# Kernel optimization log

Measured on AMD Instinct MI355X. Metric: run time of the kernel, lower is better.

The kernel has to match this reference:

```python
import jax, jax.numpy as jnp
import numpy as np

N = 100000   # nodes
E = 1600000  # edges (avg in-degree 16)
D = 64       # feature dim (dim_in = dim_out)


def setup_inputs() -> dict:
    key = jax.random.key(0)
    k1, k2, k3, k4, k5, k6 = jax.random.split(key, 6)
    h = jax.random.normal(k1, (N, D), dtype=jnp.float32)
    src = jax.random.randint(k2, (E,), 0, N, dtype=jnp.int32)
    dst = jax.random.randint(k3, (E,), 0, N, dtype=jnp.int32)
    scale = 1.0 / np.sqrt(D).astype(np.float32)
    W1 = jax.random.normal(k4, (D, D), dtype=jnp.float32) * scale  # Linear(dim_in, dim_out, bias=False)
    W2 = jax.random.normal(k5, (D, D), dtype=jnp.float32) * scale  # Linear(dim_out, dim_out, bias=True)
    b2 = jax.random.normal(k6, (D,), dtype=jnp.float32) * scale
    return {"h": h, "src": src, "dst": dst, "W1": W1, "W2": W2, "b2": b2}


def reference(h, src, dst, W1, W2, b2):
    # GINConv with 'max' aggregation, eps = 0 (DGL default, not learned):
    #   out = MLP( h + max_{(u->v) in E} h[u] )
    msgs = h[src]  # [E, D] gather of source features
    agg = jax.ops.segment_max(msgs, dst, num_segments=N)  # [N, D]
    # Nodes with no in-edges: DGL's max-reduce yields zeros, segment_max yields -inf.
    deg = jax.ops.segment_sum(jnp.ones((E,), dtype=h.dtype), dst, num_segments=N)  # [N]
    agg = jnp.where(deg[:, None] > 0, agg, jnp.zeros((), dtype=h.dtype))
    x = h + agg                       # (1 + eps) * h_dst + agg, eps = 0
    y = jnp.maximum(x @ W1.T, 0.0)    # Linear(no bias) + ReLU
    return y @ W2.T + b2              # Linear(bias)
```

## Files before the change

kernel.cpp:

```cpp
#include <hip/hip_runtime.h>
#include <math.h>

#define NN 100000
#define EE 1600000
#define D 64

#define CSH 9
#define CSIZE 512
#define NCB 196
#define CAPC 8800
#define GCS 16
#define BSH 7
#define BSIZE 128
#define NBUK 782
#define AST 65

#define EPB 2048
#define NCHUNK ((EE + EPB - 1) / EPB)
#define KPER (EPB / 256)
#define GRID 1024


__device__ __forceinline__ unsigned short encbf(float x) {
    unsigned int b = __float_as_uint(x);
    unsigned short u = (unsigned short)((b + 0x7FFFu + ((b >> 16) & 1u)) >> 16);
    return u ^ ((u & 0x8000u) ? 0xFFFFu : 0x8000u);
}

__device__ __forceinline__ unsigned int pkmax(unsigned int a, unsigned int b) {
    unsigned int d;
    asm("v_pk_max_u16 %0, %1, %2" : "=v"(d) : "v"(a), "v"(b));
    return d;
}

__global__ void __launch_bounds__(256) kAP2(const float* __restrict__ h,
                                            unsigned short* __restrict__ hb,
                                            const float* __restrict__ W1, float* __restrict__ W1T,
                                            const float* __restrict__ W2, float* __restrict__ W2T,
                                            const int* __restrict__ src, const int* __restrict__ dst,
                                            int* __restrict__ gcurC, int* __restrict__ bdataC) {
    __shared__ int lcnt[NCB];
    __shared__ int lofs[NCB];
    __shared__ int gb[NCB];
    __shared__ int lcur2[NCB];
    __shared__ unsigned int ent[EPB];
    __shared__ unsigned char bkb[EPB];
    const int t = threadIdx.x;
    const int b = blockIdx.x;

    if (b < NCHUNK) {
        for (int i = t; i < NCB; i += 256) lcnt[i] = 0;
        __syncthreads();
        const int e0 = b * EPB;
        int es[KPER], ed[KPER];
#pragma unroll
        for (int k = 0; k < KPER; k++) {
            int e = e0 + k * 256 + t;
            int d = -1, s = 0;
            if (e < EE) {
                d = dst[e];
                s = src[e];
                atomicAdd(&lcnt[d >> CSH], 1);
            }
            ed[k] = d; es[k] = s;
        }
        __syncthreads();
        if (t < NCB) lofs[t] = lcnt[t];
        __syncthreads();
        for (int s = 1; s < NCB; s <<= 1) {
            int v = 0;
            if (t < NCB) { v = lofs[t]; if (t >= s) v += lofs[t - s]; }
            __syncthreads();
            if (t < NCB) lofs[t] = v;
            __syncthreads();
        }
        if (t < NCB) {
            int c = lcnt[t];
            int ex = lofs[t] - c;
            lcur2[t] = ex;
            lofs[t] = ex;
            gb[t] = c ? atomicAdd(&gcurC[t * GCS], c) : 0;
        }
        __syncthreads();
#pragma unroll
        for (int k = 0; k < KPER; k++) {
            if (ed[k] >= 0) {
                int bk = ed[k] >> CSH;
                int p = atomicAdd(&lcur2[bk], 1);
                ent[p] = ((unsigned)es[k] << CSH) | (unsigned)(ed[k] & (CSIZE - 1));
                bkb[p] = (unsigned char)bk;
            }
        }
        __syncthreads();
        const int tot = (e0 + EPB <= EE) ? EPB : (EE - e0);
        for (int i = t; i < tot; i += 256) {
            int bk = bkb[i];
            int p = gb[bk] + (i - lofs[bk]);
            if (p < CAPC) bdataC[bk * CAPC + p] = (int)ent[i];
        }
    }

    const int gid = b * 256 + t;
    const int gsz = gridDim.x * 256;
    const float4* h4 = (const float4*)h;
    ushort4* hb4 = (ushort4*)hb;
    for (int idx = gid; idx < NN * D / 4; idx += gsz) {
        float4 v = h4[idx];
        ushort4 r;
        r.x = encbf(v.x); r.y = encbf(v.y); r.z = encbf(v.z); r.w = encbf(v.w);
        hb4[idx] = r;
    }
    if (gid < D * D) {
        int k = gid >> 6, j = gid & 63;
        W1T[gid] = W1[j * D + k];
        W2T[gid] = W2[j * D + k];
    }
}

__global__ void __launch_bounds__(512) kC3(const float* __restrict__ h,
                                           const unsigned short* __restrict__ hb,
                                           const int* __restrict__ gcurC,
                                           const int* __restrict__ bdataC,
                                           const float* __restrict__ W1T,
                                           const float* __restrict__ W2T,
                                           const float* __restrict__ b2,
                                           float* __restrict__ out) {
    __shared__ unsigned int acc[BSIZE * AST];
    __shared__ int deg[BSIZE];
    __shared__ int scn[BSIZE];
    __shared__ int cur[BSIZE];
    float* fac = (float*)acc;
    unsigned int* elist = acc;
    const int t = threadIdx.x;
    const int b = blockIdx.x;
    const int cb = b >> 2;
    const unsigned int sub = (unsigned)(b & 3);
    int cnt = gcurC[cb * GCS];
    if (cnt > CAPC) cnt = CAPC;
    const int cbase = cb * CAPC;

    if (t < BSIZE) deg[t] = 0;
    __syncthreads();
    for (int i = t; i < cnt; i += 512) {
        unsigned int e = (unsigned)bdataC[cbase + i];
        if (((e >> BSH) & 3u) == sub) atomicAdd(&deg[e & (BSIZE - 1)], 1);
    }
    __syncthreads();
    if (t < BSIZE) scn[t] = deg[t];
    __syncthreads();
    for (int s = 1; s < BSIZE; s <<= 1) {
        int v = 0;
        if (t < BSIZE) { v = scn[t]; if (t >= s) v += scn[t - s]; }
        __syncthreads();
        if (t < BSIZE) scn[t] = v;
        __syncthreads();
    }
    if (t < BSIZE) cur[t] = scn[t] - deg[t];
    __syncthreads();
    for (int i = t; i < cnt; i += 512) {
        unsigned int e = (unsigned)bdataC[cbase + i];
        if (((e >> BSH) & 3u) == sub) {
            int pos = atomicAdd(&cur[e & (BSIZE - 1)], 1);
            elist[pos] = e >> CSH;
        }
    }
    __syncthreads();

    const int wave = t >> 6, lane = t & 63;
    const int oct = lane >> 3;
    const int fbyte = (lane & 7) * 16;
    const char* hbB = (const char*)hb;
    unsigned int m[2][4];
#pragma unroll
    for (int p = 0; p < 2; ++p)
#pragma unroll
        for (int c = 0; c < 4; ++c) m[p][c] = 0u;

#pragma unroll
    for (int p = 0; p < 2; ++p) {
        const int n8 = wave * 16 + p * 8 + oct;
        const int dg = deg[n8];
        const int ofs = scn[n8] - dg;
        int md = dg;
        md = max(md, __shfl_xor(md, 8));
        md = max(md, __shfl_xor(md, 16));
        md = max(md, __shfl_xor(md, 32));
        for (int r0 = 0; r0 < md; r0 += 8) {
            uint4 u[8];
#pragma unroll
            for (int g = 0; g < 8; ++g) {
                int r = r0 + g;
                u[g] = make_uint4(0u, 0u, 0u, 0u);
                if (r < dg) {
                    unsigned int sidx = elist[ofs + r];
                    u[g] = *(const uint4*)(hbB + (size_t)sidx * 128 + fbyte);
                }
            }
#pragma unroll
            for (int g = 0; g < 8; ++g) {
                m[p][0] = pkmax(m[p][0], u[g].x);
                m[p][1] = pkmax(m[p][1], u[g].y);
                m[p][2] = pkmax(m[p][2], u[g].z);
                m[p][3] = pkmax(m[p][3], u[g].w);
            }
        }
    }
    __syncthreads();

#pragma unroll
    for (int p = 0; p < 2; ++p) {
        const int n8 = wave * 16 + p * 8 + oct;
        const int v = b * BSIZE + n8;
        const int f0 = (lane & 7) * 8;
        float x[8];
#pragma unroll
        for (int c = 0; c < 4; ++c) {
            unsigned int w = m[p][c];
            unsigned int klo = w & 0xFFFFu;
            unsigned int khi = w >> 16;
            float mlo = 0.0f, mhi = 0.0f;
            if (klo) {
                unsigned int bb = (klo & 0x8000u) ? (klo ^ 0x8000u) : ((~klo) & 0xFFFFu);
                mlo = __uint_as_float(bb << 16);
            }
            if (khi) {
                unsigned int bb = (khi & 0x8000u) ? (khi ^ 0x8000u) : ((~khi) & 0xFFFFu);
                mhi = __uint_as_float(bb << 16);
            }
            x[2 * c] = mlo;
            x[2 * c + 1] = mhi;
        }
        if (v < NN) {
            const float4* hp = (const float4*)(h + (size_t)v * D + f0);
            float4 a0 = hp[0], a1 = hp[1];
            x[0] += a0.x; x[1] += a0.y; x[2] += a0.z; x[3] += a0.w;
            x[4] += a1.x; x[5] += a1.y; x[6] += a1.z; x[7] += a1.w;
        } else {
#pragma unroll
            for (int j = 0; j < 8; ++j) x[j] = 0.0f;
        }
#pragma unroll
        for (int j = 0; j < 8; ++j) fac[n8 * AST + f0 + j] = x[j];
    }
    __syncthreads();

    const int n = t & (BSIZE - 1);
    const int hq = __builtin_amdgcn_readfirstlane(t >> 7);
    const float* w1 = W1T + hq * 16;
    const float* w2 = W2T + hq * 16;
    float y[16];
#pragma unroll
    for (int jj = 0; jj < 16; jj++) y[jj] = 0.0f;
#pragma unroll 8
    for (int k = 0; k < D; k++) {
        float xk = fac[n * AST + k];
#pragma unroll
        for (int jj = 0; jj < 16; jj++)
            y[jj] = fmaf(xk, w1[k * D + jj], y[jj]);
    }
#pragma unroll
    for (int jj = 0; jj < 16; jj++) y[jj] = fmaxf(y[jj], 0.0f);
    __syncthreads();
#pragma unroll
    for (int jj = 0; jj < 16; jj++) fac[n * AST + hq * 16 + jj] = y[jj];
    __syncthreads();

    float o[16];
#pragma unroll
    for (int ii = 0; ii < 16; ii++) o[ii] = b2[hq * 16 + ii];
#pragma unroll 8
    for (int j = 0; j < D; j++) {
        float yj = fac[n * AST + j];
#pragma unroll
        for (int ii = 0; ii < 16; ii++)
            o[ii] = fmaf(yj, w2[j * D + ii], o[ii]);
    }
    int v = b * BSIZE + n;
    if (v < NN) {
        float4* op = (float4*)(out + (size_t)v * D + hq * 16);
#pragma unroll
        for (int c = 0; c < 4; c++)
            op[c] = make_float4(o[4 * c], o[4 * c + 1], o[4 * c + 2], o[4 * c + 3]);
    }
}

extern "C" void kernel_launch(void* const* d_in, const int* in_sizes, int n_in,
                              void* d_out, int out_size, void* d_ws, size_t ws_size,
                              hipStream_t stream) {
    const float* h   = (const float*)d_in[0];
    const int*   src = (const int*)d_in[1];
    const int*   dst = (const int*)d_in[2];
    const float* W1  = (const float*)d_in[3];
    const float* W2  = (const float*)d_in[4];
    const float* b2  = (const float*)d_in[5];
    float* out = (float*)d_out;

    int* ws = (int*)d_ws;
    int* gcurC  = ws;
    int* bdataC = ws + NCB * GCS;
    float* W1T = (float*)(ws + NCB * GCS + NCB * CAPC);
    float* W2T = W1T + D * D;
    unsigned short* hb = (unsigned short*)(W2T + D * D);

    hipMemsetAsync(gcurC, 0, NCB * GCS * sizeof(int), stream);
    kAP2<<<GRID, 256, 0, stream>>>(h, hb, W1, W1T, W2, W2T, src, dst, gcurC, bdataC);
    kC3<<<NBUK, 512, 0, stream>>>(h, hb, gcurC, bdataC, W1T, W2T, b2, out);
}
```

Before: 180.7 us.

## Fuse bucketing and aggregation kernels with an atomic grid barrier

```diff
diff --git a/kernel.cpp b/kernel.cpp
--- a/kernel.cpp
+++ b/kernel.cpp
@@ -15,10 +15,10 @@
 #define NBUK 782
 #define AST 65
 
+#define NTHR 512
 #define EPB 2048
 #define NCHUNK ((EE + EPB - 1) / EPB)
-#define KPER (EPB / 256)
-#define GRID 1024
+#define KPER (EPB / NTHR)
 
 
 __device__ __forceinline__ unsigned short encbf(float x) {
@@ -33,36 +33,41 @@
     return d;
 }
 
-__global__ void __launch_bounds__(256) kAP2(const float* __restrict__ h,
-                                            unsigned short* __restrict__ hb,
-                                            const float* __restrict__ W1, float* __restrict__ W1T,
-                                            const float* __restrict__ W2, float* __restrict__ W2T,
-                                            const int* __restrict__ src, const int* __restrict__ dst,
-                                            int* __restrict__ gcurC, int* __restrict__ bdataC) {
-    __shared__ int lcnt[NCB];
-    __shared__ int lofs[NCB];
-    __shared__ int gb[NCB];
-    __shared__ int lcur2[NCB];
-    __shared__ unsigned int ent[EPB];
-    __shared__ unsigned char bkb[EPB];
+__global__ void __launch_bounds__(NTHR) kFused(
+    const float* __restrict__ h, const int* __restrict__ src, const int* __restrict__ dst,
+    const float* __restrict__ W1, const float* __restrict__ W2, const float* __restrict__ b2,
+    float* __restrict__ out, int* __restrict__ done, int* __restrict__ gcurC,
+    int* __restrict__ bdataC, float* __restrict__ W1T, float* __restrict__ W2T,
+    unsigned short* __restrict__ hb) {
+    __shared__ unsigned int acc[BSIZE * AST];
+    __shared__ int deg[BSIZE];
+    __shared__ int scn[BSIZE];
+    __shared__ int cur[BSIZE];
     const int t = threadIdx.x;
     const int b = blockIdx.x;
 
-    if (b < NCHUNK) {
-        for (int i = t; i < NCB; i += 256) lcnt[i] = 0;
+    {
+        unsigned int* ent = acc;
+        unsigned char* bkb = (unsigned char*)(acc + EPB);
+        int* lcnt  = (int*)(acc + EPB + EPB / 4);
+        int* lofs  = lcnt + NCB;
+        int* gb    = lofs + NCB;
+        int* lcur2 = gb + NCB;
+
+        for (int i = t; i < NCB; i += NTHR) lcnt[i] = 0;
         __syncthreads();
         const int e0 = b * EPB;
         int es[KPER], ed[KPER];
 #pragma unroll
         for (int k = 0; k < KPER; k++) {
-            int e = e0 + k * 256 + t;
-            int d = -1, s = 0;
+            int e = e0 + k * NTHR + t;
+            int dd = -1, s = 0;
             if (e < EE) {
-                d = dst[e];
+                dd = dst[e];
                 s = src[e];
-                atomicAdd(&lcnt[d >> CSH], 1);
-            }
-            ed[k] = d; es[k] = s;
+                atomicAdd(&lcnt[dd >> CSH], 1);
+            }
+            ed[k] = dd; es[k] = s;
         }
         __syncthreads();
         if (t < NCB) lofs[t] = lcnt[t];
@@ -93,46 +98,47 @@
         }
         __syncthreads();
         const int tot = (e0 + EPB <= EE) ? EPB : (EE - e0);
-        for (int i = t; i < tot; i += 256) {
+        for (int i = t; i < tot; i += NTHR) {
             int bk = bkb[i];
             int p = gb[bk] + (i - lofs[bk]);
             if (p < CAPC) bdataC[bk * CAPC + p] = (int)ent[i];
         }
     }
 
-    const int gid = b * 256 + t;
-    const int gsz = gridDim.x * 256;
-    const float4* h4 = (const float4*)h;
-    ushort4* hb4 = (ushort4*)hb;
-    for (int idx = gid; idx < NN * D / 4; idx += gsz) {
-        float4 v = h4[idx];
-        ushort4 r;
-        r.x = encbf(v.x); r.y = encbf(v.y); r.z = encbf(v.z); r.w = encbf(v.w);
-        hb4[idx] = r;
-    }
-    if (gid < D * D) {
-        int k = gid >> 6, j = gid & 63;
-        W1T[gid] = W1[j * D + k];
-        W2T[gid] = W2[j * D + k];
-    }
-}
-
-__global__ void __launch_bounds__(512) kC3(const float* __restrict__ h,
-                                           const unsigned short* __restrict__ hb,
-                                           const int* __restrict__ gcurC,
-                                           const int* __restrict__ bdataC,
-                                           const float* __restrict__ W1T,
-                                           const float* __restrict__ W2T,
-                                           const float* __restrict__ b2,
-                                           float* __restrict__ out) {
-    __shared__ unsigned int acc[BSIZE * AST];
-    __shared__ int deg[BSIZE];
-    __shared__ int scn[BSIZE];
-    __shared__ int cur[BSIZE];
+    {
+        const int gid = b * NTHR + t;
+        const int gsz = NCHUNK * NTHR;
+        const float4* h4 = (const float4*)h;
+        ushort4* hb4 = (ushort4*)hb;
+        for (int idx = gid; idx < NN * D / 4; idx += gsz) {
+            float4 v = h4[idx];
+            ushort4 r;
+            r.x = encbf(v.x); r.y = encbf(v.y); r.z = encbf(v.z); r.w = encbf(v.w);
+            hb4[idx] = r;
+        }
+        if (gid < D * D) {
+            int k = gid >> 6, j = gid & 63;
+            W1T[gid] = W1[j * D + k];
+            W2T[gid] = W2[j * D + k];
+        }
+    }
+
+    __syncthreads();
+    if (t == 0) {
+        __threadfence();
+        atomicAdd(done, 1);
+        int spins = 0;
+        while (__hip_atomic_load(done, __ATOMIC_ACQUIRE, __HIP_MEMORY_SCOPE_AGENT)
+               < NCHUNK) {
+            __builtin_amdgcn_s_sleep(2);
+            if (++spins > (1 << 22)) break;
+        }
+        __threadfence();
+    }
+    __syncthreads();
+
     float* fac = (float*)acc;
     unsigned int* elist = acc;
-    const int t = threadIdx.x;
-    const int b = blockIdx.x;
     const int cb = b >> 2;
     const unsigned int sub = (unsigned)(b & 3);
     int cnt = gcurC[cb * GCS];
@@ -141,7 +147,7 @@
 
     if (t < BSIZE) deg[t] = 0;
     __syncthreads();
-    for (int i = t; i < cnt; i += 512) {
+    for (int i = t; i < cnt; i += NTHR) {
         unsigned int e = (unsigned)bdataC[cbase + i];
         if (((e >> BSH) & 3u) == sub) atomicAdd(&deg[e & (BSIZE - 1)], 1);
     }
@@ -157,7 +163,7 @@
     }
     if (t < BSIZE) cur[t] = scn[t] - deg[t];
     __syncthreads();
-    for (int i = t; i < cnt; i += 512) {
+    for (int i = t; i < cnt; i += NTHR) {
         unsigned int e = (unsigned)bdataC[cbase + i];
         if (((e >> BSH) & 3u) == sub) {
             int pos = atomicAdd(&cur[e & (BSIZE - 1)], 1);
@@ -296,13 +302,14 @@
     float* out = (float*)d_out;
 
     int* ws = (int*)d_ws;
-    int* gcurC  = ws;
-    int* bdataC = ws + NCB * GCS;
-    float* W1T = (float*)(ws + NCB * GCS + NCB * CAPC);
+    int* done   = ws;
+    int* gcurC  = ws + 16;
+    int* bdataC = ws + 16 + NCB * GCS;
+    float* W1T = (float*)(ws + 16 + NCB * GCS + NCB * CAPC);
     float* W2T = W1T + D * D;
     unsigned short* hb = (unsigned short*)(W2T + D * D);
 
-    hipMemsetAsync(gcurC, 0, NCB * GCS * sizeof(int), stream);
-    kAP2<<<GRID, 256, 0, stream>>>(h, hb, W1, W1T, W2, W2T, src, dst, gcurC, bdataC);
-    kC3<<<NBUK, 512, 0, stream>>>(h, hb, gcurC, bdataC, W1T, W2T, b2, out);
+    hipMemsetAsync(ws, 0, (16 + NCB * GCS) * sizeof(int), stream);
+    kFused<<<NCHUNK, NTHR, 0, stream>>>(h, src, dst, W1, W2, b2, out,
+                                        done, gcurC, bdataC, W1T, W2T, hb);
 }
```

New measurement: 402.6 us. +122.8%, slower.

## Sort nodes by degree within block and cache edge list in registers

Applied to the files above, without the earlier changes.

```diff
diff --git a/kernel.cpp b/kernel.cpp
--- a/kernel.cpp
+++ b/kernel.cpp
@@ -19,6 +19,7 @@
 #define NCHUNK ((EE + EPB - 1) / EPB)
 #define KPER (EPB / 256)
 #define GRID 1024
+#define KREG 18
 
 
 __device__ __forceinline__ unsigned short encbf(float x) {
@@ -129,6 +130,7 @@
     __shared__ int deg[BSIZE];
     __shared__ int scn[BSIZE];
     __shared__ int cur[BSIZE];
+    __shared__ int perm[BSIZE];
     float* fac = (float*)acc;
     unsigned int* elist = acc;
     const int t = threadIdx.x;
@@ -139,12 +141,18 @@
     if (cnt > CAPC) cnt = CAPC;
     const int cbase = cb * CAPC;
 
+    unsigned int ebuf[KREG];
+#pragma unroll
+    for (int k = 0; k < KREG; k++) {
+        int i = t + k * 512;
+        ebuf[k] = (i < cnt) ? (unsigned)bdataC[cbase + i] : 0u;
+        if (i >= cnt || ((ebuf[k] >> BSH) & 3u) != sub) ebuf[k] = 0xFFFFFFFFu;
+    }
     if (t < BSIZE) deg[t] = 0;
     __syncthreads();
-    for (int i = t; i < cnt; i += 512) {
-        unsigned int e = (unsigned)bdataC[cbase + i];
-        if (((e >> BSH) & 3u) == sub) atomicAdd(&deg[e & (BSIZE - 1)], 1);
-    }
+#pragma unroll
+    for (int k = 0; k < KREG; k++)
+        if (ebuf[k] != 0xFFFFFFFFu) atomicAdd(&deg[ebuf[k] & (BSIZE - 1)], 1);
     __syncthreads();
     if (t < BSIZE) scn[t] = deg[t];
     __syncthreads();
@@ -155,11 +163,21 @@
         if (t < BSIZE) scn[t] = v;
         __syncthreads();
     }
-    if (t < BSIZE) cur[t] = scn[t] - deg[t];
-    __syncthreads();
-    for (int i = t; i < cnt; i += 512) {
-        unsigned int e = (unsigned)bdataC[cbase + i];
-        if (((e >> BSH) & 3u) == sub) {
+    if (t < BSIZE) {
+        cur[t] = scn[t] - deg[t];
+        int d = deg[t];
+        int r = 0;
+        for (int j = 0; j < BSIZE; ++j) {
+            int dj = deg[j];
+            r += (dj < d) || (dj == d && j < t);
+        }
+        perm[r] = t;
+    }
+    __syncthreads();
+#pragma unroll
+    for (int k = 0; k < KREG; k++) {
+        unsigned int e = ebuf[k];
+        if (e != 0xFFFFFFFFu) {
             int pos = atomicAdd(&cur[e & (BSIZE - 1)], 1);
             elist[pos] = e >> CSH;
         }
@@ -171,6 +189,7 @@
     const int fbyte = (lane & 7) * 16;
     const char* hbB = (const char*)hb;
     unsigned int m[2][4];
+    int n8v[2];
 #pragma unroll
     for (int p = 0; p < 2; ++p)
 #pragma unroll
@@ -178,7 +197,8 @@
 
 #pragma unroll
     for (int p = 0; p < 2; ++p) {
-        const int n8 = wave * 16 + p * 8 + oct;
+        const int n8 = perm[wave * 16 + p * 8 + oct];
+        n8v[p] = n8;
         const int dg = deg[n8];
         const int ofs = scn[n8] - dg;
         int md = dg;
@@ -209,7 +229,7 @@
 
 #pragma unroll
     for (int p = 0; p < 2; ++p) {
-        const int n8 = wave * 16 + p * 8 + oct;
+        const int n8 = n8v[p];
         const int v = b * BSIZE + n8;
         const int f0 = (lane & 7) * 8;
         float x[8];
```

Measured after the change: 189.2 us. +4.7%, slower.

## Remap kC3 blocks so sibling sub-buckets share an XCD, widen gather unroll

Applied to the files above, without the earlier changes.

```diff
diff --git a/kernel.cpp b/kernel.cpp
--- a/kernel.cpp
+++ b/kernel.cpp
@@ -19,6 +19,7 @@
 #define NCHUNK ((EE + EPB - 1) / EPB)
 #define KPER (EPB / 256)
 #define GRID 1024
+#define CGRID 800
 
 
 __device__ __forceinline__ unsigned short encbf(float x) {
@@ -125,6 +126,12 @@
                                            const float* __restrict__ W2T,
                                            const float* __restrict__ b2,
                                            float* __restrict__ out) {
+    const int i = blockIdx.x;
+    const int x = i & 7, k0 = i >> 3;
+    const int q = x + 8 * (k0 >> 2);
+    const int b = q * 4 + (k0 & 3);
+    if (b >= NBUK) return;
+
     __shared__ unsigned int acc[BSIZE * AST];
     __shared__ int deg[BSIZE];
     __shared__ int scn[BSIZE];
@@ -132,7 +139,6 @@
     float* fac = (float*)acc;
     unsigned int* elist = acc;
     const int t = threadIdx.x;
-    const int b = blockIdx.x;
     const int cb = b >> 2;
     const unsigned int sub = (unsigned)(b & 3);
     int cnt = gcurC[cb * GCS];
@@ -141,8 +147,8 @@
 
     if (t < BSIZE) deg[t] = 0;
     __syncthreads();
-    for (int i = t; i < cnt; i += 512) {
-        unsigned int e = (unsigned)bdataC[cbase + i];
+    for (int i2 = t; i2 < cnt; i2 += 512) {
+        unsigned int e = (unsigned)bdataC[cbase + i2];
         if (((e >> BSH) & 3u) == sub) atomicAdd(&deg[e & (BSIZE - 1)], 1);
     }
     __syncthreads();
@@ -157,8 +163,8 @@
     }
     if (t < BSIZE) cur[t] = scn[t] - deg[t];
     __syncthreads();
-    for (int i = t; i < cnt; i += 512) {
-        unsigned int e = (unsigned)bdataC[cbase + i];
+    for (int i2 = t; i2 < cnt; i2 += 512) {
+        unsigned int e = (unsigned)bdataC[cbase + i2];
         if (((e >> BSH) & 3u) == sub) {
             int pos = atomicAdd(&cur[e & (BSIZE - 1)], 1);
             elist[pos] = e >> CSH;
@@ -185,10 +191,10 @@
         md = max(md, __shfl_xor(md, 8));
         md = max(md, __shfl_xor(md, 16));
         md = max(md, __shfl_xor(md, 32));
-        for (int r0 = 0; r0 < md; r0 += 8) {
-            uint4 u[8];
-#pragma unroll
-            for (int g = 0; g < 8; ++g) {
+        for (int r0 = 0; r0 < md; r0 += 16) {
+            uint4 u[16];
+#pragma unroll
+            for (int g = 0; g < 16; ++g) {
                 int r = r0 + g;
                 u[g] = make_uint4(0u, 0u, 0u, 0u);
                 if (r < dg) {
@@ -197,11 +203,13 @@
                 }
             }
 #pragma unroll
-            for (int g = 0; g < 8; ++g) {
-                m[p][0] = pkmax(m[p][0], u[g].x);
-                m[p][1] = pkmax(m[p][1], u[g].y);
-                m[p][2] = pkmax(m[p][2], u[g].z);
-                m[p][3] = pkmax(m[p][3], u[g].w);
+            for (int g = 0; g < 16; ++g) {
+                if (r0 + g < dg) {
+                    m[p][0] = pkmax(m[p][0], u[g].x);
+                    m[p][1] = pkmax(m[p][1], u[g].y);
+                    m[p][2] = pkmax(m[p][2], u[g].z);
+                    m[p][3] = pkmax(m[p][3], u[g].w);
+                }
             }
         }
     }
@@ -212,7 +220,7 @@
         const int n8 = wave * 16 + p * 8 + oct;
         const int v = b * BSIZE + n8;
         const int f0 = (lane & 7) * 8;
-        float x[8];
+        float xx[8];
 #pragma unroll
         for (int c = 0; c < 4; ++c) {
             unsigned int w = m[p][c];
@@ -227,20 +235,20 @@
                 unsigned int bb = (khi & 0x8000u) ? (khi ^ 0x8000u) : ((~khi) & 0xFFFFu);
                 mhi = __uint_as_float(bb << 16);
             }
-            x[2 * c] = mlo;
-            x[2 * c + 1] = mhi;
+            xx[2 * c] = mlo;
+            xx[2 * c + 1] = mhi;
         }
         if (v < NN) {
             const float4* hp = (const float4*)(h + (size_t)v * D + f0);
             float4 a0 = hp[0], a1 = hp[1];
-            x[0] += a0.x; x[1] += a0.y; x[2] += a0.z; x[3] += a0.w;
-            x[4] += a1.x; x[5] += a1.y; x[6] += a1.z; x[7] += a1.w;
+            xx[0] += a0.x; xx[1] += a0.y; xx[2] += a0.z; xx[3] += a0.w;
+            xx[4] += a1.x; xx[5] += a1.y; xx[6] += a1.z; xx[7] += a1.w;
         } else {
 #pragma unroll
-            for (int j = 0; j < 8; ++j) x[j] = 0.0f;
-        }
-#pragma unroll
-        for (int j = 0; j < 8; ++j) fac[n8 * AST + f0 + j] = x[j];
+            for (int j = 0; j < 8; ++j) xx[j] = 0.0f;
+        }
+#pragma unroll
+        for (int j = 0; j < 8; ++j) fac[n8 * AST + f0 + j] = xx[j];
     }
     __syncthreads();
 
@@ -304,5 +312,5 @@
 
     hipMemsetAsync(gcurC, 0, NCB * GCS * sizeof(int), stream);
     kAP2<<<GRID, 256, 0, stream>>>(h, hb, W1, W1T, W2, W2T, src, dst, gcurC, bdataC);
-    kC3<<<NBUK, 512, 0, stream>>>(h, hb, gcurC, bdataC, W1T, W2T, b2, out);
-}
+    kC3<<<CGRID, 512, 0, stream>>>(h, hb, gcurC, bdataC, W1T, W2T, b2, out);
+}
```

Result: no change. 183.6 us (+1.6%).
